# Optimization experiments

Measured on AMD Instinct MI355X. Metric: run time of the kernel, lower is better.

The kernel has to match this reference:

```python
import jax, jax.numpy as jnp
import numpy as np

S, T, H, D = 4096, 4096, 16, 64
N_EMBD = H * D

def setup_inputs() -> dict:
    key = jax.random.key(0)
    kq, kk, kv, kw = jax.random.split(key, 4)
    q = jax.random.normal(kq, (S, H, D), dtype=jnp.float32)
    k = jax.random.normal(kk, (T, H, D), dtype=jnp.float32)
    v = jax.random.normal(kv, (T, H, D), dtype=jnp.float32)
    # GPT-2 style init: std = 0.02 / sqrt(2 * n_layer), n_layer = 24
    W_proj = jax.random.normal(kw, (N_EMBD, N_EMBD), dtype=jnp.float32) * (0.02 / np.sqrt(2 * 24))
    return {"q": q, "k": k, "v": v, "W_proj": W_proj}

def reference(q, k, v, W_proj):
    s, h, d = q.shape
    t = k.shape[0]
    # causal bias: mask positions where query index < key index (future keys)
    causal_bias = (jnp.arange(s)[:, None] < jnp.arange(t)[None, :]).astype(jnp.float32) * -10000.0
    scale = 1.0 / jnp.sqrt(jnp.float32(d))
    # [h, s, t] scores in fp32 (matches original .astype(jnp.float32))
    scores = jnp.einsum('shd,thd->hst', q, k).astype(jnp.float32) * scale + causal_bias
    attn = jax.nn.softmax(scores, axis=-1).astype(q.dtype)
    # dropout p=0 / inference -> identity
    out = jnp.einsum('hst,thd->shd', attn, v).reshape(s, h * d)
    # nn.Linear (no bias) vmapped over tokens: y = x @ W.T
    return out @ W_proj.T
```

## Files before the change

### kernel.cpp

```cpp
#include <hip/hip_runtime.h>

#define S_LEN 4096
#define NH 16
#define DH 64
#define NE 1024

typedef __bf16 bf16_t;
typedef __bf16 bf16x8 __attribute__((ext_vector_type(8)));
typedef __bf16 bf16x4 __attribute__((ext_vector_type(4)));
typedef __bf16 bf16x2 __attribute__((ext_vector_type(2)));
typedef float  f32x4  __attribute__((ext_vector_type(4)));

#define QSCALE 0.180336879f

__global__ __launch_bounds__(256) void pack_all(const float* __restrict__ q,
                                                const float* __restrict__ k,
                                                const float* __restrict__ w,
                                                const float* __restrict__ v,
                                                bf16_t* __restrict__ qb,
                                                bf16_t* __restrict__ kb,
                                                bf16_t* __restrict__ wb,
                                                bf16_t* __restrict__ vt) {
    __shared__ bf16_t tile[64][65];
    const int bid = blockIdx.x;
    if (bid < 4096) {
        const int tid = bid * 256 + threadIdx.x;
        const int e = tid * 4;
        const int s = e >> 10;
        const int c = e & (NE - 1);
        const int h = c >> 6;
        const int d = c & (DH - 1);
        const int o = (h * S_LEN + s) * DH + d;
        float4 qv = *(const float4*)(q + e);
        float4 kv = *(const float4*)(k + e);
        bf16x4 qo, ko;
        qo[0] = (bf16_t)(qv.x * QSCALE); qo[1] = (bf16_t)(qv.y * QSCALE);
        qo[2] = (bf16_t)(qv.z * QSCALE); qo[3] = (bf16_t)(qv.w * QSCALE);
        ko[0] = (bf16_t)kv.x; ko[1] = (bf16_t)kv.y; ko[2] = (bf16_t)kv.z; ko[3] = (bf16_t)kv.w;
        *(bf16x4*)(qb + o) = qo;
        *(bf16x4*)(kb + o) = ko;
        if (tid < (NE * NE / 4)) {
            float4 wv = *(const float4*)(w + tid * 4);
            bf16x4 wo;
            wo[0] = (bf16_t)wv.x; wo[1] = (bf16_t)wv.y; wo[2] = (bf16_t)wv.z; wo[3] = (bf16_t)wv.w;
            *(bf16x4*)(wb + tid * 4) = wo;
        }
    } else {
        const int vb = bid - 4096;
        const int h  = vb >> 6;
        const int t0 = (vb & 63) * 64;
        const int r  = threadIdx.x >> 6;
        const int cl = threadIdx.x & 63;
#pragma unroll
        for (int rep = 0; rep < 16; ++rep) {
            int i = rep * 4 + r;
            tile[cl][i] = (bf16_t)v[(t0 + i) * NE + h * DH + cl];
        }
        __syncthreads();
        const int r2  = threadIdx.x >> 5;
        const int cl2 = (threadIdx.x & 31) * 2;
        const int ip = (cl2 & 32) + ((cl2 >> 2) & 1) * 16 + ((cl2 >> 4) & 1) * 8 +
                       ((cl2 >> 3) & 1) * 4 + (cl2 & 3);
#pragma unroll
        for (int rep = 0; rep < 8; ++rep) {
            int d = rep * 8 + r2;
            bf16x2 out;
            out[0] = tile[d][ip];
            out[1] = tile[d][ip + 1];
            *(bf16x2*)(vt + (h * DH + d) * S_LEN + t0 + cl2) = out;
        }
    }
}

__global__ __launch_bounds__(512, 4) void attn(const bf16_t* __restrict__ qb,
                                               const bf16_t* __restrict__ kb,
                                               const bf16_t* __restrict__ vt,
                                               float* __restrict__ po,
                                               float* __restrict__ ls) {
    __shared__ __align__(16) bf16_t kbuf[2][64 * 72];
    __shared__ __align__(16) bf16_t vbuf[2][64 * 72];

    const int tid  = threadIdx.x;
    const int wave = tid >> 6;
    const int lane = tid & 63;
    const int l15  = lane & 15;
    const int quad = lane >> 4;
    const int h = blockIdx.x;
    const int x = blockIdx.y;

    const int sA = x;
    const int sB = 31 - x;
    const int n0 = x + 1;
    const int b1 = sB + 1;
    const int N  = 33;

    const bf16_t* __restrict__ qh = qb + h * (S_LEN * DH);
    const bf16_t* __restrict__ kh = kb + h * (S_LEN * DH);
    const bf16_t* __restrict__ vh = vt + h * (DH * S_LEN);

    const int row0 = tid >> 3;
    const int tc8  = (tid & 7) * 8;
    const int stg  = row0 * 72 + tc8;
    const int frg  = l15 * 72 + quad * 8;

    f32x4 o_acc[4];
    f32x4 rs;
    bf16x8 qA[2];
    bf16x8 ones;
#pragma unroll
    for (int e = 0; e < 8; ++e) ones[e] = (bf16_t)1.0f;
    int s0 = sA * 128 + wave * 16;

    auto load_q = [&](int s0_) {
#pragma unroll
        for (int dc = 0; dc < 2; ++dc)
            qA[dc] = *(const bf16x8*)(qh + (s0_ + l15) * DH + dc * 32 + quad * 8);
    };
    auto reset_acc = [&]() {
#pragma unroll
        for (int db = 0; db < 4; ++db) o_acc[db] = (f32x4){0.f, 0.f, 0.f, 0.f};
        rs = (f32x4){0.f, 0.f, 0.f, 0.f};
    };
    auto epilogue = [&](int s0_, int slot) {
        float* poz = po + (size_t)(slot * NH + h) * S_LEN * DH;
#pragma unroll
        for (int db = 0; db < 4; ++db)
#pragma unroll
            for (int r = 0; r < 4; ++r)
                poz[(s0_ + quad * 4 + r) * DH + db * 16 + l15] = o_acc[db][r];
        if (l15 == 0) {
            float* lsz = ls + (size_t)(slot * NH + h) * S_LEN;
#pragma unroll
            for (int r = 0; r < 4; ++r) lsz[s0_ + quad * 4 + r] = rs[r];
        }
    };

    load_q(s0);
    reset_acc();

    {
        bf16x8 kr = *(const bf16x8*)(kh + row0 * DH + tc8);
        bf16x8 vr = *(const bf16x8*)(vh + row0 * S_LEN + tc8);
        *(bf16x8*)(kbuf[0] + stg) = kr;
        *(bf16x8*)(vbuf[0] + stg) = vr;
    }
    __syncthreads();

#pragma unroll 2
    for (int j = 0; j < N; ++j) {
        if (j == n0) {
            epilogue(s0, 0);
            s0 = sB * 128 + wave * 16;
            load_q(s0);
            reset_acc();
        }
        const int t0 = (j < n0 ? j : b1 + (j - n0)) * 64;
        const bf16_t* kb_ = kbuf[j & 1];
        const bf16_t* vb_ = vbuf[j & 1];

        bf16x8 krn, vrn;
        const bool pf = (j + 1 < N);
        if (pf) {
            const int jn = j + 1;
            const int tn = (jn < n0 ? jn : b1 + (jn - n0)) * 64;
            krn = *(const bf16x8*)(kh + (tn + row0) * DH + tc8);
            vrn = *(const bf16x8*)(vh + row0 * S_LEN + tn + tc8);
        }

        if (t0 <= s0 + 15) {
            f32x4 c_[4];
#pragma unroll
            for (int ch = 0; ch < 4; ++ch) {
                bf16x8 kB0 = *(const bf16x8*)(kb_ + frg + ch * (16 * 72));
                bf16x8 kB1 = *(const bf16x8*)(kb_ + frg + ch * (16 * 72) + 32);
                f32x4 zr = (f32x4){0.f, 0.f, 0.f, 0.f};
                zr = __builtin_amdgcn_mfma_f32_16x16x32_bf16(kB0, qA[0], zr, 0, 0, 0);
                zr = __builtin_amdgcn_mfma_f32_16x16x32_bf16(kB1, qA[1], zr, 0, 0, 0);
                c_[ch] = zr;
            }

            const int query = s0 + l15;
            float p[4][4];
#pragma unroll
            for (int ch = 0; ch < 4; ++ch) {
                if (t0 + ch * 16 <= s0 + 15) {
                    const bool edge = (t0 + ch * 16 + 15 > s0);
#pragma unroll
                    for (int r = 0; r < 4; ++r) {
                        float cc = c_[ch][r];
                        if (edge) {
                            int key = t0 + ch * 16 + quad * 4 + r;
                            if (key > query) cc = -INFINITY;
                        }
                        p[ch][r] = exp2f(cc);
                    }
                } else {
#pragma unroll
                    for (int r = 0; r < 4; ++r) p[ch][r] = 0.0f;
                }
            }

            bf16x8 pA[2];
#pragma unroll
            for (int kc = 0; kc < 2; ++kc) {
                bf16x8 t;
                t[0] = (bf16_t)p[2 * kc][0];     t[1] = (bf16_t)p[2 * kc][1];
                t[2] = (bf16_t)p[2 * kc][2];     t[3] = (bf16_t)p[2 * kc][3];
                t[4] = (bf16_t)p[2 * kc + 1][0]; t[5] = (bf16_t)p[2 * kc + 1][1];
                t[6] = (bf16_t)p[2 * kc + 1][2]; t[7] = (bf16_t)p[2 * kc + 1][3];
                pA[kc] = t;
            }

            rs = __builtin_amdgcn_mfma_f32_16x16x32_bf16(pA[0], ones, rs, 0, 0, 0);
            rs = __builtin_amdgcn_mfma_f32_16x16x32_bf16(pA[1], ones, rs, 0, 0, 0);

#pragma unroll
            for (int db = 0; db < 4; ++db) {
#pragma unroll
                for (int kc = 0; kc < 2; ++kc) {
                    bf16x8 vB = *(const bf16x8*)(vb_ + frg + db * (16 * 72) + kc * 32);
                    o_acc[db] = __builtin_amdgcn_mfma_f32_16x16x32_bf16(pA[kc], vB, o_acc[db], 0, 0, 0);
                }
            }
        }

        if (pf) {
            *(bf16x8*)(kbuf[(j + 1) & 1] + stg) = krn;
            *(bf16x8*)(vbuf[(j + 1) & 1] + stg) = vrn;
        }
        __syncthreads();
    }

    epilogue(s0, 1);
}

__global__ __launch_bounds__(256) void combine(const float* __restrict__ po,
                                               const float* __restrict__ ls,
                                               bf16_t* __restrict__ xb) {
    const int idx = blockIdx.x * 256 + threadIdx.x;
    const int row = idx >> 8;
    const int c   = (idx & 255) * 4;
    const int h   = c >> 6;
    const int d   = c & 63;
    const size_t base0 = (size_t)(h) * S_LEN * DH + row * DH + d;
    const size_t base1 = (size_t)(NH + h) * S_LEN * DH + row * DH + d;
    float4 o0 = *(const float4*)(po + base0);
    float4 o1 = *(const float4*)(po + base1);
    float l = ls[(size_t)h * S_LEN + row] + ls[(size_t)(NH + h) * S_LEN + row];
    float inv = 1.0f / l;
    bf16x4 out;
    out[0] = (bf16_t)((o0.x + o1.x) * inv);
    out[1] = (bf16_t)((o0.y + o1.y) * inv);
    out[2] = (bf16_t)((o0.z + o1.z) * inv);
    out[3] = (bf16_t)((o0.w + o1.w) * inv);
    *(bf16x4*)(xb + (size_t)row * NE + c) = out;
}

__global__ __launch_bounds__(256, 4) void proj(const bf16_t* __restrict__ xb,
                                               const bf16_t* __restrict__ wb,
                                               float* __restrict__ y) {
    __shared__ __align__(16) bf16_t wbuf[2][64 * 72];
    const int tid  = threadIdx.x;
    const int wave = tid >> 6;
    const int lane = tid & 63;
    const int l15  = lane & 15;
    const int quad = lane >> 4;
    const int m0 = blockIdx.x * 128 + wave * 32;
    const int n0 = blockIdx.y * 64;

    const int row0 = tid >> 3;
    const int tc8  = (tid & 7) * 8;

    f32x4 acc[2][4];
#pragma unroll
    for (int g = 0; g < 2; ++g)
#pragma unroll
        for (int nb = 0; nb < 4; ++nb) acc[g][nb] = (f32x4){0.f, 0.f, 0.f, 0.f};

    {
        bf16x8 wr0 = *(const bf16x8*)(wb + (n0 + row0) * NE + tc8);
        bf16x8 wr1 = *(const bf16x8*)(wb + (n0 + row0 + 32) * NE + tc8);
        *(bf16x8*)(wbuf[0] + row0 * 72 + tc8) = wr0;
        *(bf16x8*)(wbuf[0] + (row0 + 32) * 72 + tc8) = wr1;
    }
    bf16x8 a[2][2];
#pragma unroll
    for (int g = 0; g < 2; ++g)
#pragma unroll
        for (int kc = 0; kc < 2; ++kc)
            a[g][kc] = *(const bf16x8*)(xb + (m0 + g * 16 + l15) * NE + kc * 32 + quad * 8);
    __syncthreads();

    for (int kt = 0; kt < 16; ++kt) {
        const bf16_t* wb_ = wbuf[kt & 1];
        const bool pf = (kt + 1 < 16);
        bf16x8 wr0, wr1, an[2][2];
        if (pf) {
            const int kn = (kt + 1) * 64;
            wr0 = *(const bf16x8*)(wb + (n0 + row0) * NE + kn + tc8);
            wr1 = *(const bf16x8*)(wb + (n0 + row0 + 32) * NE + kn + tc8);
#pragma unroll
            for (int g = 0; g < 2; ++g)
#pragma unroll
                for (int kc = 0; kc < 2; ++kc)
                    an[g][kc] = *(const bf16x8*)(xb + (m0 + g * 16 + l15) * NE + kn + kc * 32 + quad * 8);
        }

#pragma unroll
        for (int nb = 0; nb < 4; ++nb)
#pragma unroll
            for (int kc = 0; kc < 2; ++kc) {
                bf16x8 b = *(const bf16x8*)(wb_ + (nb * 16 + l15) * 72 + kc * 32 + quad * 8);
#pragma unroll
                for (int g = 0; g < 2; ++g)
                    acc[g][nb] = __builtin_amdgcn_mfma_f32_16x16x32_bf16(a[g][kc], b, acc[g][nb], 0, 0, 0);
            }

        if (pf) {
            *(bf16x8*)(wbuf[(kt + 1) & 1] + row0 * 72 + tc8) = wr0;
            *(bf16x8*)(wbuf[(kt + 1) & 1] + (row0 + 32) * 72 + tc8) = wr1;
#pragma unroll
            for (int g = 0; g < 2; ++g)
#pragma unroll
                for (int kc = 0; kc < 2; ++kc) a[g][kc] = an[g][kc];
        }
        __syncthreads();
    }

#pragma unroll
    for (int g = 0; g < 2; ++g)
#pragma unroll
        for (int nb = 0; nb < 4; ++nb)
#pragma unroll
            for (int r = 0; r < 4; ++r)
                y[(m0 + g * 16 + quad * 4 + r) * NE + n0 + nb * 16 + l15] = acc[g][nb][r];
}

extern "C" void kernel_launch(void* const* d_in, const int* in_sizes, int n_in,
                              void* d_out, int out_size, void* d_ws, size_t ws_size,
                              hipStream_t stream) {
    const float* q = (const float*)d_in[0];
    const float* k = (const float*)d_in[1];
    const float* v = (const float*)d_in[2];
    const float* w = (const float*)d_in[3];
    float* y = (float*)d_out;

    bf16_t* ws = (bf16_t*)d_ws;
    bf16_t* qb = ws;
    bf16_t* kb = qb + 4 * 1024 * 1024;
    bf16_t* vt = kb + 4 * 1024 * 1024;
    bf16_t* wb = vt + 4 * 1024 * 1024;
    bf16_t* xb = wb + 1024 * 1024;
    float*  po = (float*)(xb + 4 * 1024 * 1024);
    float*  ls = po + (size_t)2 * NH * S_LEN * DH;

    pack_all<<<dim3(4096 + 1024), dim3(256), 0, stream>>>(q, k, w, v, qb, kb, wb, vt);
    attn<<<dim3(NH, 32), dim3(512), 0, stream>>>(qb, kb, vt, po, ls);
    combine<<<dim3(4096), dim3(256), 0, stream>>>(po, ls, xb);
    proj<<<dim3(S_LEN / 128, NE / 64), dim3(256), 0, stream>>>(xb, wb, y);
}
```

Baseline: 194.9 us.

## Read K and V fragments directly from global memory instead of LDS staging

Removes the double-buffered shared-memory staging of K and V tiles, along with the per-iteration barrier. Each wave now loads its MFMA operand fragments straight from global memory, relying on the cache for reuse across the 8 waves. This drops LDS traffic and synchronisation, but multiplies global and L2 load requests, since every wave refetches the same tile. It also loses the software prefetch that overlapped the next tile's loads with compute.

```diff
diff --git a/kernel.cpp b/kernel.cpp
--- a/kernel.cpp
+++ b/kernel.cpp
@@ -77,9 +77,6 @@
                                                const bf16_t* __restrict__ vt,
                                                float* __restrict__ po,
                                                float* __restrict__ ls) {
-    __shared__ __align__(16) bf16_t kbuf[2][64 * 72];
-    __shared__ __align__(16) bf16_t vbuf[2][64 * 72];
-
     const int tid  = threadIdx.x;
     const int wave = tid >> 6;
     const int lane = tid & 63;
@@ -98,11 +95,6 @@
     const bf16_t* __restrict__ kh = kb + h * (S_LEN * DH);
     const bf16_t* __restrict__ vh = vt + h * (DH * S_LEN);
 
-    const int row0 = tid >> 3;
-    const int tc8  = (tid & 7) * 8;
-    const int stg  = row0 * 72 + tc8;
-    const int frg  = l15 * 72 + quad * 8;
-
     f32x4 o_acc[4];
     f32x4 rs;
     bf16x8 qA[2];
@@ -137,14 +129,6 @@
 
     load_q(s0);
     reset_acc();
-
-    {
-        bf16x8 kr = *(const bf16x8*)(kh + row0 * DH + tc8);
-        bf16x8 vr = *(const bf16x8*)(vh + row0 * S_LEN + tc8);
-        *(bf16x8*)(kbuf[0] + stg) = kr;
-        *(bf16x8*)(vbuf[0] + stg) = vr;
-    }
-    __syncthreads();
 
 #pragma unroll 2
     for (int j = 0; j < N; ++j) {
@@ -155,24 +139,16 @@
             reset_acc();
         }
         const int t0 = (j < n0 ? j : b1 + (j - n0)) * 64;
-        const bf16_t* kb_ = kbuf[j & 1];
-        const bf16_t* vb_ = vbuf[j & 1];
-
-        bf16x8 krn, vrn;
-        const bool pf = (j + 1 < N);
-        if (pf) {
-            const int jn = j + 1;
-            const int tn = (jn < n0 ? jn : b1 + (jn - n0)) * 64;
-            krn = *(const bf16x8*)(kh + (tn + row0) * DH + tc8);
-            vrn = *(const bf16x8*)(vh + row0 * S_LEN + tn + tc8);
-        }
 
         if (t0 <= s0 + 15) {
+            const bf16_t* kt = kh + t0 * DH;
+            const bf16_t* vp = vh + t0;
+
             f32x4 c_[4];
 #pragma unroll
             for (int ch = 0; ch < 4; ++ch) {
-                bf16x8 kB0 = *(const bf16x8*)(kb_ + frg + ch * (16 * 72));
-                bf16x8 kB1 = *(const bf16x8*)(kb_ + frg + ch * (16 * 72) + 32);
+                bf16x8 kB0 = *(const bf16x8*)(kt + (ch * 16 + l15) * DH + quad * 8);
+                bf16x8 kB1 = *(const bf16x8*)(kt + (ch * 16 + l15) * DH + 32 + quad * 8);
                 f32x4 zr = (f32x4){0.f, 0.f, 0.f, 0.f};
                 zr = __builtin_amdgcn_mfma_f32_16x16x32_bf16(kB0, qA[0], zr, 0, 0, 0);
                 zr = __builtin_amdgcn_mfma_f32_16x16x32_bf16(kB1, qA[1], zr, 0, 0, 0);
@@ -218,17 +194,11 @@
             for (int db = 0; db < 4; ++db) {
 #pragma unroll
                 for (int kc = 0; kc < 2; ++kc) {
-                    bf16x8 vB = *(const bf16x8*)(vb_ + frg + db * (16 * 72) + kc * 32);
+                    bf16x8 vB = *(const bf16x8*)(vp + (db * 16 + l15) * S_LEN + kc * 32 + quad * 8);
                     o_acc[db] = __builtin_amdgcn_mfma_f32_16x16x32_bf16(pA[kc], vB, o_acc[db], 0, 0, 0);
                 }
             }
         }
-
-        if (pf) {
-            *(bf16x8*)(kbuf[(j + 1) & 1] + stg) = krn;
-            *(bf16x8*)(vbuf[(j + 1) & 1] + stg) = vrn;
-        }
-        __syncthreads();
     }
 
     epilogue(s0, 1);
```

Result: slower. 357.4 us (+83.4%).

## Give each attention wave two 16-row query groups with 256-thread blocks

Applied to the files above, without the earlier changes.

Halves the attention block to 4 waves. Each wave now handles 32 query rows as two 16-row groups, so every K and V fragment read from LDS feeds MFMAs for both groups. Each thread stages two rows of K/V per tile instead of one. It also skips MFMAs for causally masked 16-key chunks per group. This should cut LDS traffic per MFMA and sync overhead per row, at the cost of more registers per thread and fewer waves to hide latency.

```diff
diff --git a/kernel.cpp b/kernel.cpp
--- a/kernel.cpp
+++ b/kernel.cpp
@@ -72,7 +72,7 @@
     }
 }
 
-__global__ __launch_bounds__(512, 4) void attn(const bf16_t* __restrict__ qb,
+__global__ __launch_bounds__(256, 4) void attn(const bf16_t* __restrict__ qb,
                                                const bf16_t* __restrict__ kb,
                                                const bf16_t* __restrict__ vt,
                                                float* __restrict__ po,
@@ -103,35 +103,44 @@
     const int stg  = row0 * 72 + tc8;
     const int frg  = l15 * 72 + quad * 8;
 
-    f32x4 o_acc[4];
-    f32x4 rs;
-    bf16x8 qA[2];
+    f32x4 o_acc[2][4];
+    f32x4 rs[2];
+    bf16x8 qA[2][2];
     bf16x8 ones;
 #pragma unroll
     for (int e = 0; e < 8; ++e) ones[e] = (bf16_t)1.0f;
-    int s0 = sA * 128 + wave * 16;
+    int s0 = sA * 128 + wave * 32;
 
     auto load_q = [&](int s0_) {
 #pragma unroll
-        for (int dc = 0; dc < 2; ++dc)
-            qA[dc] = *(const bf16x8*)(qh + (s0_ + l15) * DH + dc * 32 + quad * 8);
+        for (int g = 0; g < 2; ++g)
+#pragma unroll
+            for (int dc = 0; dc < 2; ++dc)
+                qA[g][dc] = *(const bf16x8*)(qh + (s0_ + g * 16 + l15) * DH + dc * 32 + quad * 8);
     };
     auto reset_acc = [&]() {
 #pragma unroll
-        for (int db = 0; db < 4; ++db) o_acc[db] = (f32x4){0.f, 0.f, 0.f, 0.f};
-        rs = (f32x4){0.f, 0.f, 0.f, 0.f};
+        for (int g = 0; g < 2; ++g) {
+#pragma unroll
+            for (int db = 0; db < 4; ++db) o_acc[g][db] = (f32x4){0.f, 0.f, 0.f, 0.f};
+            rs[g] = (f32x4){0.f, 0.f, 0.f, 0.f};
+        }
     };
     auto epilogue = [&](int s0_, int slot) {
         float* poz = po + (size_t)(slot * NH + h) * S_LEN * DH;
 #pragma unroll
-        for (int db = 0; db < 4; ++db)
-#pragma unroll
-            for (int r = 0; r < 4; ++r)
-                poz[(s0_ + quad * 4 + r) * DH + db * 16 + l15] = o_acc[db][r];
+        for (int g = 0; g < 2; ++g)
+#pragma unroll
+            for (int db = 0; db < 4; ++db)
+#pragma unroll
+                for (int r = 0; r < 4; ++r)
+                    poz[(s0_ + g * 16 + quad * 4 + r) * DH + db * 16 + l15] = o_acc[g][db][r];
         if (l15 == 0) {
             float* lsz = ls + (size_t)(slot * NH + h) * S_LEN;
 #pragma unroll
-            for (int r = 0; r < 4; ++r) lsz[s0_ + quad * 4 + r] = rs[r];
+            for (int g = 0; g < 2; ++g)
+#pragma unroll
+                for (int r = 0; r < 4; ++r) lsz[s0_ + g * 16 + quad * 4 + r] = rs[g][r];
         }
     };
 
@@ -139,10 +148,14 @@
     reset_acc();
 
     {
-        bf16x8 kr = *(const bf16x8*)(kh + row0 * DH + tc8);
-        bf16x8 vr = *(const bf16x8*)(vh + row0 * S_LEN + tc8);
-        *(bf16x8*)(kbuf[0] + stg) = kr;
-        *(bf16x8*)(vbuf[0] + stg) = vr;
+        bf16x8 kr0 = *(const bf16x8*)(kh + row0 * DH + tc8);
+        bf16x8 kr1 = *(const bf16x8*)(kh + (row0 + 32) * DH + tc8);
+        bf16x8 vr0 = *(const bf16x8*)(vh + row0 * S_LEN + tc8);
+        bf16x8 vr1 = *(const bf16x8*)(vh + (row0 + 32) * S_LEN + tc8);
+        *(bf16x8*)(kbuf[0] + stg) = kr0;
+        *(bf16x8*)(kbuf[0] + stg + 32 * 72) = kr1;
+        *(bf16x8*)(vbuf[0] + stg) = vr0;
+        *(bf16x8*)(vbuf[0] + stg + 32 * 72) = vr1;
     }
     __syncthreads();
 
@@ -150,7 +163,7 @@
     for (int j = 0; j < N; ++j) {
         if (j == n0) {
             epilogue(s0, 0);
-            s0 = sB * 128 + wave * 16;
+            s0 = sB * 128 + wave * 32;
             load_q(s0);
             reset_acc();
         }
@@ -158,75 +171,102 @@
         const bf16_t* kb_ = kbuf[j & 1];
         const bf16_t* vb_ = vbuf[j & 1];
 
-        bf16x8 krn, vrn;
+        bf16x8 kr0n, kr1n, vr0n, vr1n;
         const bool pf = (j + 1 < N);
         if (pf) {
             const int jn = j + 1;
             const int tn = (jn < n0 ? jn : b1 + (jn - n0)) * 64;
-            krn = *(const bf16x8*)(kh + (tn + row0) * DH + tc8);
-            vrn = *(const bf16x8*)(vh + row0 * S_LEN + tn + tc8);
-        }
-
-        if (t0 <= s0 + 15) {
-            f32x4 c_[4];
+            kr0n = *(const bf16x8*)(kh + (tn + row0) * DH + tc8);
+            kr1n = *(const bf16x8*)(kh + (tn + row0 + 32) * DH + tc8);
+            vr0n = *(const bf16x8*)(vh + row0 * S_LEN + tn + tc8);
+            vr1n = *(const bf16x8*)(vh + (row0 + 32) * S_LEN + tn + tc8);
+        }
+
+        if (t0 <= s0 + 31) {
+            f32x4 c_[2][4];
 #pragma unroll
             for (int ch = 0; ch < 4; ++ch) {
-                bf16x8 kB0 = *(const bf16x8*)(kb_ + frg + ch * (16 * 72));
-                bf16x8 kB1 = *(const bf16x8*)(kb_ + frg + ch * (16 * 72) + 32);
-                f32x4 zr = (f32x4){0.f, 0.f, 0.f, 0.f};
-                zr = __builtin_amdgcn_mfma_f32_16x16x32_bf16(kB0, qA[0], zr, 0, 0, 0);
-                zr = __builtin_amdgcn_mfma_f32_16x16x32_bf16(kB1, qA[1], zr, 0, 0, 0);
-                c_[ch] = zr;
-            }
-
-            const int query = s0 + l15;
-            float p[4][4];
-#pragma unroll
-            for (int ch = 0; ch < 4; ++ch) {
-                if (t0 + ch * 16 <= s0 + 15) {
-                    const bool edge = (t0 + ch * 16 + 15 > s0);
-#pragma unroll
-                    for (int r = 0; r < 4; ++r) {
-                        float cc = c_[ch][r];
-                        if (edge) {
-                            int key = t0 + ch * 16 + quad * 4 + r;
-                            if (key > query) cc = -INFINITY;
+                if (t0 + ch * 16 <= s0 + 31) {
+                    bf16x8 kB0 = *(const bf16x8*)(kb_ + frg + ch * (16 * 72));
+                    bf16x8 kB1 = *(const bf16x8*)(kb_ + frg + ch * (16 * 72) + 32);
+#pragma unroll
+                    for (int g = 0; g < 2; ++g) {
+                        if (t0 + ch * 16 <= s0 + g * 16 + 15) {
+                            f32x4 zr = (f32x4){0.f, 0.f, 0.f, 0.f};
+                            zr = __builtin_amdgcn_mfma_f32_16x16x32_bf16(kB0, qA[g][0], zr, 0, 0, 0);
+                            zr = __builtin_amdgcn_mfma_f32_16x16x32_bf16(kB1, qA[g][1], zr, 0, 0, 0);
+                            c_[g][ch] = zr;
                         }
-                        p[ch][r] = exp2f(cc);
                     }
-                } else {
-#pragma unroll
-                    for (int r = 0; r < 4; ++r) p[ch][r] = 0.0f;
                 }
             }
 
-            bf16x8 pA[2];
-#pragma unroll
-            for (int kc = 0; kc < 2; ++kc) {
-                bf16x8 t;
-                t[0] = (bf16_t)p[2 * kc][0];     t[1] = (bf16_t)p[2 * kc][1];
-                t[2] = (bf16_t)p[2 * kc][2];     t[3] = (bf16_t)p[2 * kc][3];
-                t[4] = (bf16_t)p[2 * kc + 1][0]; t[5] = (bf16_t)p[2 * kc + 1][1];
-                t[6] = (bf16_t)p[2 * kc + 1][2]; t[7] = (bf16_t)p[2 * kc + 1][3];
-                pA[kc] = t;
-            }
-
-            rs = __builtin_amdgcn_mfma_f32_16x16x32_bf16(pA[0], ones, rs, 0, 0, 0);
-            rs = __builtin_amdgcn_mfma_f32_16x16x32_bf16(pA[1], ones, rs, 0, 0, 0);
-
-#pragma unroll
-            for (int db = 0; db < 4; ++db) {
+            bf16x8 pA[2][2];
+#pragma unroll
+            for (int g = 0; g < 2; ++g) {
+                const int slim  = s0 + g * 16;
+                const int query = slim + l15;
+                float p[4][4];
+#pragma unroll
+                for (int ch = 0; ch < 4; ++ch) {
+                    if (t0 + ch * 16 <= slim + 15) {
+                        const bool edge = (t0 + ch * 16 + 15 > slim);
+#pragma unroll
+                        for (int r = 0; r < 4; ++r) {
+                            float cc = c_[g][ch][r];
+                            if (edge) {
+                                int key = t0 + ch * 16 + quad * 4 + r;
+                                if (key > query) cc = -INFINITY;
+                            }
+                            p[ch][r] = exp2f(cc);
+                        }
+                    } else {
+#pragma unroll
+                        for (int r = 0; r < 4; ++r) p[ch][r] = 0.0f;
+                    }
+                }
 #pragma unroll
                 for (int kc = 0; kc < 2; ++kc) {
-                    bf16x8 vB = *(const bf16x8*)(vb_ + frg + db * (16 * 72) + kc * 32);
-                    o_acc[db] = __builtin_amdgcn_mfma_f32_16x16x32_bf16(pA[kc], vB, o_acc[db], 0, 0, 0);
+                    bf16x8 t;
+                    t[0] = (bf16_t)p[2 * kc][0];     t[1] = (bf16_t)p[2 * kc][1];
+                    t[2] = (bf16_t)p[2 * kc][2];     t[3] = (bf16_t)p[2 * kc][3];
+                    t[4] = (bf16_t)p[2 * kc + 1][0]; t[5] = (bf16_t)p[2 * kc + 1][1];
+                    t[6] = (bf16_t)p[2 * kc + 1][2]; t[7] = (bf16_t)p[2 * kc + 1][3];
+                    pA[g][kc] = t;
                 }
             }
+
+#pragma unroll
+            for (int g = 0; g < 2; ++g)
+#pragma unroll
+                for (int kc = 0; kc < 2; ++kc)
+                    if (t0 + kc * 32 <= s0 + g * 16 + 15)
+                        rs[g] = __builtin_amdgcn_mfma_f32_16x16x32_bf16(pA[g][kc], ones, rs[g], 0, 0, 0);
+
+#pragma unroll
+            for (int db = 0; db < 4; ++db) {
+                bf16x8 vB0 = *(const bf16x8*)(vb_ + frg + db * (16 * 72));
+#pragma unroll
+                for (int g = 0; g < 2; ++g)
+                    if (t0 <= s0 + g * 16 + 15)
+                        o_acc[g][db] = __builtin_amdgcn_mfma_f32_16x16x32_bf16(pA[g][0], vB0, o_acc[g][db], 0, 0, 0);
+                if (t0 + 32 <= s0 + 31) {
+                    bf16x8 vB1 = *(const bf16x8*)(vb_ + frg + db * (16 * 72) + 32);
+#pragma unroll
+                    for (int g = 0; g < 2; ++g)
+                        if (t0 + 32 <= s0 + g * 16 + 15)
+                            o_acc[g][db] = __builtin_amdgcn_mfma_f32_16x16x32_bf16(pA[g][1], vB1, o_acc[g][db], 0, 0, 0);
+                }
+            }
         }
 
         if (pf) {
-            *(bf16x8*)(kbuf[(j + 1) & 1] + stg) = krn;
-            *(bf16x8*)(vbuf[(j + 1) & 1] + stg) = vrn;
+            bf16_t* kd = kbuf[(j + 1) & 1];
+            bf16_t* vd = vbuf[(j + 1) & 1];
+            *(bf16x8*)(kd + stg) = kr0n;
+            *(bf16x8*)(kd + stg + 32 * 72) = kr1n;
+            *(bf16x8*)(vd + stg) = vr0n;
+            *(bf16x8*)(vd + stg + 32 * 72) = vr1n;
         }
         __syncthreads();
     }
@@ -355,7 +395,7 @@
     float*  ls = po + (size_t)2 * NH * S_LEN * DH;
 
     pack_all<<<dim3(4096 + 1024), dim3(256), 0, stream>>>(q, k, w, v, qb, kb, wb, vt);
-    attn<<<dim3(NH, 32), dim3(512), 0, stream>>>(qb, kb, vt, po, ls);
+    attn<<<dim3(NH, 32), dim3(256), 0, stream>>>(qb, kb, vt, po, ls);
     combine<<<dim3(4096), dim3(256), 0, stream>>>(po, ls, xb);
     proj<<<dim3(S_LEN / 128, NE / 64), dim3(256), 0, stream>>>(xb, wb, y);
 }
```

New measurement: 312.9 us. 60.5% more time.
